# Kernel tuning notes

Hardware: AMD Instinct MI355X
Metric: run time of the kernel (lower is better)

The kernel has to match this reference:

```python
import jax, jax.numpy as jnp
import numpy as np

# Static config (matches init_kwargs / chosen geometry)
DIM, HEADS, WS, SHIFT = 96, 3, 7, 3
H, W = 56, 56
B = 64
N = WS * WS
HID = int(DIM * 4.0)
EPS = 1e-5


def _rel_tables():
    # relative_coords_table: (1, 2*WS-1, 2*WS-1, 2), log-spaced coords in [-1,1]
    c = np.arange(-(WS - 1), WS, dtype=np.float32)
    tab = np.stack(np.meshgrid(c, c, indexing='ij'), axis=-1)[None]
    tab = tab / (WS - 1) * 8.0
    tab = np.sign(tab) * np.log2(np.abs(tab) + 1.0) / np.log2(8.0)
    # relative_position_index: (N, N) int
    coords = np.stack(np.meshgrid(np.arange(WS), np.arange(WS), indexing='ij'))
    cf = coords.reshape(2, -1)
    rel = (cf[:, :, None] - cf[:, None, :]).transpose(1, 2, 0).astype(np.int64)
    rel[..., 0] += WS - 1
    rel[..., 1] += WS - 1
    rel[..., 0] *= 2 * WS - 1
    return jnp.asarray(tab), jnp.asarray(rel.sum(-1))

_TABLE, _RPI = _rel_tables()


def _shift_mask():
    # standard SW-MSA mask: (num_windows, N, N), 0 / -100
    img = np.zeros((1, H, W, 1), dtype=np.float32)
    cnt = 0
    segs = (slice(0, -WS), slice(-WS, -SHIFT), slice(-SHIFT, None))
    for hs in segs:
        for ws_ in segs:
            img[:, hs, ws_, :] = cnt
            cnt += 1
    mw = img.reshape(1, H // WS, WS, W // WS, WS, 1).transpose(0, 1, 3, 2, 4, 5).reshape(-1, N)
    am = mw[:, None, :] - mw[:, :, None]
    return jnp.asarray(np.where(am != 0, -100.0, 0.0).astype(np.float32))


def _ln(x, g, b):
    mu = x.mean(-1, keepdims=True)
    var = x.var(-1, keepdims=True)
    return (x - mu) * jax.lax.rsqrt(var + EPS) * g + b


def setup_inputs() -> dict:
    key = jax.random.key(0)
    ks = jax.random.split(key, 8)
    s = 0.02
    return {
        'x': jax.random.normal(ks[0], (B, H * W, DIM), jnp.float32),
        'attn_mask': _shift_mask(),
        'qkv_w': jax.random.normal(ks[1], (3 * DIM, DIM), jnp.float32) * s,
        'q_bias': jnp.zeros((DIM,), jnp.float32),
        'v_bias': jnp.zeros((DIM,), jnp.float32),
        'logit_scale': jnp.full((HEADS, 1, 1), np.log(10.0), jnp.float32),
        'cpb_w1': jax.random.normal(ks[2], (512, 2), jnp.float32) * s,
        'cpb_b1': jnp.zeros((512,), jnp.float32),
        'cpb_w2': jax.random.normal(ks[3], (HEADS, 512), jnp.float32) * s,
        'proj_w': jax.random.normal(ks[4], (DIM, DIM), jnp.float32) * s,
        'proj_b': jnp.zeros((DIM,), jnp.float32),
        'norm1_g': jnp.ones((DIM,), jnp.float32),
        'norm1_b': jnp.zeros((DIM,), jnp.float32),
        'fc1_w': jax.random.normal(ks[5], (HID, DIM), jnp.float32) * s,
        'fc1_b': jnp.zeros((HID,), jnp.float32),
        'fc2_w': jax.random.normal(ks[6], (DIM, HID), jnp.float32) * s,
        'fc2_b': jnp.zeros((DIM,), jnp.float32),
        'norm2_g': jnp.ones((DIM,), jnp.float32),
        'norm2_b': jnp.zeros((DIM,), jnp.float32),
    }


def reference(x, attn_mask, qkv_w, q_bias, v_bias, logit_scale, cpb_w1, cpb_b1,
              cpb_w2, proj_w, proj_b, norm1_g, norm1_b, fc1_w, fc1_b, fc2_w,
              fc2_b, norm2_g, norm2_b):
    Bx, L, C = x.shape
    d = C // HEADS
    nH, nWd = H // WS, W // WS
    shortcut = x

    xi = x.reshape(Bx, H, W, C)
    xi = jnp.roll(xi, (-SHIFT, -SHIFT), axis=(1, 2))
    # window partition -> (Bx*nH*nWd, N, C)
    xw = xi.reshape(Bx, nH, WS, nWd, WS, C).transpose(0, 1, 3, 2, 4, 5).reshape(-1, N, C)

    # qkv with q/v bias only (k bias fixed to zero)
    qkv_bias = jnp.concatenate([q_bias, jnp.zeros_like(v_bias), v_bias])
    qkv = (xw @ qkv_w.T + qkv_bias).reshape(-1, N, 3, HEADS, d).transpose(2, 0, 3, 1, 4)
    q, k, v = qkv[0], qkv[1], qkv[2]  # (B_, h, N, d)

    # cosine attention with clamped learnable temperature
    qn = q / jnp.maximum(jnp.linalg.norm(q, axis=-1, keepdims=True), 1e-12)
    kn = k / jnp.maximum(jnp.linalg.norm(k, axis=-1, keepdims=True), 1e-12)
    attn = jnp.einsum('bhnd,bhmd->bhnm', qn, kn)
    scale = jnp.exp(jnp.minimum(logit_scale, jnp.log(jnp.float32(100.0))))
    attn = attn * scale

    # continuous relative position bias via cpb_mlp
    tab = jax.nn.gelu(_TABLE @ cpb_w1.T + cpb_b1, approximate=False) @ cpb_w2.T
    tab = tab.reshape(-1, HEADS)
    rpb = tab[_RPI.reshape(-1)].reshape(N, N, HEADS).transpose(2, 0, 1)
    attn = attn + (16.0 * jax.nn.sigmoid(rpb))[None]

    # shift mask
    nWin = attn_mask.shape[0]
    attn = attn.reshape(-1, nWin, HEADS, N, N) + attn_mask[None, :, None]
    attn = jax.nn.softmax(attn.reshape(-1, HEADS, N, N), axis=-1)

    out = jnp.einsum('bhnm,bhmd->bnhd', attn, v).reshape(-1, N, C)
    out = out @ proj_w.T + proj_b

    # window reverse + un-shift
    out = out.reshape(Bx, nH, nWd, WS, WS, C).transpose(0, 1, 3, 2, 4, 5).reshape(Bx, H, W, C)
    out = jnp.roll(out, (SHIFT, SHIFT), axis=(1, 2)).reshape(Bx, L, C)

    # SwinV2 post-norm residuals
    x1 = shortcut + _ln(out, norm1_g, norm1_b)
    h = jax.nn.gelu(x1 @ fc1_w.T + fc1_b, approximate=False) @ fc2_w.T + fc2_b
    return x1 + _ln(h, norm2_g, norm2_b)
```

## Files before the change

### kernel.cpp

```cpp
#include <hip/hip_runtime.h>
#include <math.h>

#define BATCH 64
#define HW 56
#define CDIM 96
#define NHEADS 3
#define WSZ 7
#define NTOK 49
#define SHIFT_ 3
#define NWIN_TOT 4096
#define HID 384
#define NTOKENS (BATCH * HW * HW)
#define LN100 4.6051702f

typedef __attribute__((ext_vector_type(8))) short bf16x8;
typedef __attribute__((ext_vector_type(8))) _Float16 f16x8;
typedef __attribute__((ext_vector_type(4))) float f32x4;

__device__ inline f32x4 mfma16(bf16x8 a, bf16x8 b, f32x4 c) {
  return __builtin_amdgcn_mfma_f32_16x16x32_bf16(a, b, c, 0, 0, 0);
}
__device__ inline f32x4 mfma16h(f16x8 a, f16x8 b, f32x4 c) {
  return __builtin_amdgcn_mfma_f32_16x16x32_f16(a, b, c, 0, 0, 0);
}

__device__ inline unsigned short f2b(float f) {
  unsigned u = __float_as_uint(f);
  unsigned r = (u + 0x7FFFu + ((u >> 16) & 1u)) >> 16;
  return (unsigned short)r;
}
__device__ inline float blo(unsigned u) { return __uint_as_float(u << 16); }
__device__ inline float bhi(unsigned u) { return __uint_as_float(u & 0xFFFF0000u); }
__device__ inline unsigned packb(float a, float b) {
  return (unsigned)f2b(a) | ((unsigned)f2b(b) << 16);
}
__device__ inline float gelu_f(float v) {
  float a = fabsf(v) * 0.70710678118654752f;
  float t = 1.0f / fmaf(a, 0.3275911f, 1.0f);
  float p = t * fmaf(t, fmaf(t, fmaf(t, fmaf(t, 1.061405429f, -1.453152027f),
                                     1.421413741f), -0.284496736f), 0.254829592f);
  float er = 1.0f - p * __expf(-a * a);
  er = (v < 0.f) ? -er : er;
  return 0.5f * v * (1.0f + er);
}

__global__ __launch_bounds__(256) void wconv2_kernel(
    const float* __restrict__ qkv_w, const float* __restrict__ fc1_w,
    const float* __restrict__ fc2_w, const float* __restrict__ proj_w,
    unsigned* __restrict__ qkvf, unsigned* __restrict__ w1f,
    unsigned* __restrict__ w2f, unsigned* __restrict__ pwf) {
  int T = blockIdx.x * 256 + threadIdx.x;
  if (T < 3456) {
    int tk = T >> 6, l = T & 63;
    int n = tk / 3, ks = tk - n * 3;
    int o = n * 16 + (l & 15);
    const float* src = qkv_w + o * 96 + ks * 32 + (l >> 4) * 8;
    uint4 d;
    d.x = packb(src[0], src[1]); d.y = packb(src[2], src[3]);
    d.z = packb(src[4], src[5]); d.w = packb(src[6], src[7]);
    *(uint4*)&qkvf[(size_t)(tk * 64 + l) * 4] = d;
    return;
  }
  T -= 3456;
  if (T < 4608) {
    int tk = T >> 6, l = T & 63;
    int n = tk / 3, ks = tk - n * 3;
    int o = n * 16 + (l & 15);
    const float* src = fc1_w + o * 96 + ks * 32 + (l >> 4) * 8;
    uint4 d;
    d.x = packb(src[0], src[1]); d.y = packb(src[2], src[3]);
    d.z = packb(src[4], src[5]); d.w = packb(src[6], src[7]);
    *(uint4*)&w1f[(size_t)(tk * 64 + l) * 4] = d;
    return;
  }
  T -= 4608;
  if (T < 4608) {
    int tk = T >> 6, l = T & 63;
    int n = tk / 12, ks = tk - n * 12;
    int o = n * 16 + (l & 15);
    const float* src = fc2_w + o * 384 + ks * 32 + (l >> 4) * 8;
    uint4 d;
    d.x = packb(src[0], src[1]); d.y = packb(src[2], src[3]);
    d.z = packb(src[4], src[5]); d.w = packb(src[6], src[7]);
    *(uint4*)&w2f[(size_t)(tk * 64 + l) * 4] = d;
    return;
  }
  T -= 4608;
  if (T < 1152) {
    int tk = T >> 6, l = T & 63;
    int n = tk / 3, ks = tk - n * 3;
    int o = n * 16 + (l & 15);
    const float* src = proj_w + o * 96 + ks * 32 + (l >> 4) * 8;
    uint4 d;
    d.x = packb(src[0], src[1]); d.y = packb(src[2], src[3]);
    d.z = packb(src[4], src[5]); d.w = packb(src[6], src[7]);
    *(uint4*)&pwf[(size_t)(tk * 64 + l) * 4] = d;
  }
}

__global__ __launch_bounds__(512) void cpb_table_kernel(
    const float* __restrict__ w1, const float* __restrict__ b1,
    const float* __restrict__ w2, float* __restrict__ tabout) {
  int tid = threadIdx.x;
  if (tid >= 169 * 3) return;
  int e = tid / 3, h = tid - e * 3;
  int i = e / 13, j = e - i * 13;
  float ti = (float)(i - 6) * (8.0f / 6.0f);
  float tj = (float)(j - 6) * (8.0f / 6.0f);
  float sx = (ti > 0.f) ? 1.f : (ti < 0.f ? -1.f : 0.f);
  float sy = (tj > 0.f) ? 1.f : (tj < 0.f ? -1.f : 0.f);
  float tx = sx * log2f(fabsf(ti) + 1.f) * (1.0f / 3.0f);
  float ty = sy * log2f(fabsf(tj) + 1.f) * (1.0f / 3.0f);
  float acc = 0.f;
  for (int jj = 0; jj < 512; ++jj) {
    float hv = tx * w1[jj * 2 + 0] + ty * w1[jj * 2 + 1] + b1[jj];
    float g = 0.5f * hv * (1.f + erff(hv * 0.70710678118654752f));
    acc += g * w2[h * 512 + jj];
  }
  tabout[e * 3 + h] = acc;
}

__global__ __launch_bounds__(256) void bias_kernel(
    const float* __restrict__ tabout, float* __restrict__ bias16) {
  int idx = blockIdx.x * 256 + threadIdx.x;
  if (idx >= NHEADS * NTOK * NTOK) return;
  int h = idx / (NTOK * NTOK);
  int rem = idx - h * NTOK * NTOK;
  int i = rem / NTOK, j = rem - i * NTOK;
  int ri = (i / WSZ) - (j / WSZ) + 6;
  int ci = (i % WSZ) - (j % WSZ) + 6;
  int e = ri * 13 + ci;
  float v = tabout[e * 3 + h];
  bias16[idx] = 16.f / (1.f + expf(-v));
}

__global__ __launch_bounds__(256) void qkv_mfma_kernel(
    const float* __restrict__ x, const unsigned* __restrict__ qkvf,
    const float* __restrict__ q_bias, const float* __restrict__ v_bias,
    const float* __restrict__ logit_scale,
    unsigned* __restrict__ qws, unsigned* __restrict__ kws,
    unsigned* __restrict__ vws) {
  __shared__ unsigned xa[64 * 52];
  int tid = threadIdx.x, lane = tid & 63, wv = tid >> 6;
  size_t tok0 = (size_t)blockIdx.x * 64;

  for (int idx = tid; idx < 3072; idx += 256) {
    int t = idx / 48, c2 = idx - t * 48;
    const float2 s = *(const float2*)(x + (tok0 + t) * 96 + c2 * 2);
    xa[t * 52 + c2] = packb(s.x, s.y);
  }
  __syncthreads();

  int c15 = lane & 15, q4 = lane >> 4;
  bf16x8 afr[3];
  #pragma unroll
  for (int k = 0; k < 3; ++k)
    afr[k] = *(const bf16x8*)&xa[(wv * 16 + c15) * 52 + k * 16 + q4 * 4];

  f32x4 acc[18];
  #pragma unroll
  for (int n = 0; n < 18; ++n) acc[n] = f32x4{0.f, 0.f, 0.f, 0.f};
  #pragma unroll
  for (int n = 0; n < 18; ++n) {
    #pragma unroll
    for (int k = 0; k < 3; ++k) {
      bf16x8 b = *(const bf16x8*)&qkvf[(size_t)((n * 3 + k) * 64 + lane) * 4];
      acc[n] = mfma16(afr[k], b, acc[n]);
    }
  }

  int tokr0 = (int)tok0 + wv * 16 + q4 * 4;
  #pragma unroll
  for (int h = 0; h < 3; ++h) {
    float sc = expf(fminf(logit_scale[h], LN100));
    {
      f32x4 a0 = acc[2 * h], a1 = acc[2 * h + 1];
      float b0 = q_bias[h * 32 + c15], b1 = q_bias[h * 32 + 16 + c15];
      unsigned pk[8];
      #pragma unroll
      for (int i = 0; i < 4; ++i) {
        float va = a0[i] + b0, vb = a1[i] + b1;
        float ss = va * va + vb * vb;
        ss += __shfl_xor(ss, 1, 64); ss += __shfl_xor(ss, 2, 64);
        ss += __shfl_xor(ss, 4, 64); ss += __shfl_xor(ss, 8, 64);
        float inv = sc / fmaxf(sqrtf(ss), 1e-12f);
        va *= inv; vb *= inv;
        float pa = __shfl_xor(va, 1, 64), pb = __shfl_xor(vb, 1, 64);
        pk[i] = packb(va, pa); pk[4 + i] = packb(vb, pb);
      }
      if (!(lane & 1)) {
        int dw0 = c15 >> 1;
        #pragma unroll
        for (int i = 0; i < 4; ++i) {
          size_t base = ((size_t)(tokr0 + i) * 3 + h) * 16;
          qws[base + dw0] = pk[i];
          qws[base + 8 + dw0] = pk[4 + i];
        }
      }
    }
    {
      f32x4 a0 = acc[6 + 2 * h], a1 = acc[7 + 2 * h];
      unsigned pk[8];
      #pragma unroll
      for (int i = 0; i < 4; ++i) {
        float va = a0[i], vb = a1[i];
        float ss = va * va + vb * vb;
        ss += __shfl_xor(ss, 1, 64); ss += __shfl_xor(ss, 2, 64);
        ss += __shfl_xor(ss, 4, 64); ss += __shfl_xor(ss, 8, 64);
        float inv = 1.f / fmaxf(sqrtf(ss), 1e-12f);
        va *= inv; vb *= inv;
        float pa = __shfl_xor(va, 1, 64), pb = __shfl_xor(vb, 1, 64);
        pk[i] = packb(va, pa); pk[4 + i] = packb(vb, pb);
      }
      if (!(lane & 1)) {
        int dw0 = c15 >> 1;
        #pragma unroll
        for (int i = 0; i < 4; ++i) {
          size_t base = ((size_t)(tokr0 + i) * 3 + h) * 16;
          kws[base + dw0] = pk[i];
          kws[base + 8 + dw0] = pk[4 + i];
        }
      }
    }
    {
      f32x4 a0 = acc[12 + 2 * h], a1 = acc[13 + 2 * h];
      float b0 = v_bias[h * 32 + c15], b1 = v_bias[h * 32 + 16 + c15];
      unsigned pk[8];
      #pragma unroll
      for (int i = 0; i < 4; ++i) {
        float va = a0[i] + b0, vb = a1[i] + b1;
        float pa = __shfl_xor(va, 1, 64), pb = __shfl_xor(vb, 1, 64);
        pk[i] = packb(va, pa); pk[4 + i] = packb(vb, pb);
      }
      if (!(lane & 1)) {
        int dw0 = c15 >> 1;
        #pragma unroll
        for (int i = 0; i < 4; ++i) {
          size_t base = ((size_t)(tokr0 + i) * 3 + h) * 16;
          vws[base + dw0] = pk[i];
          vws[base + 8 + dw0] = pk[4 + i];
        }
      }
    }
  }
}

__global__ __launch_bounds__(256) void attn_fused_kernel(
    const unsigned* __restrict__ qws, const unsigned* __restrict__ kws,
    const unsigned* __restrict__ vws, const float* __restrict__ bias16,
    const float* __restrict__ mask, const unsigned* __restrict__ pwf,
    const float* __restrict__ proj_b, const float* __restrict__ x,
    const float* __restrict__ n1g, const float* __restrict__ n1b,
    float* __restrict__ out) {
  __shared__ __align__(16) unsigned smem[12992];
  _Float16* VtS  = (_Float16*)smem;
  _Float16* Ph   = (_Float16*)((char*)smem + 13824);
  unsigned* obuf = (unsigned*)((char*)smem + 38400);
  int*      toks = (int*)((char*)smem + 51712);
  float*    ybuf = (float*)smem;

  int tid = threadIdx.x, lane = tid & 63, wv = tid >> 6;
  int c15 = lane & 15, q4 = lane >> 4;
  int win = blockIdx.x;
  int b = win >> 6, wi = win & 63, wh = wi >> 3, wcx = wi & 7;

  if (tid < 64) {
    int t = tid < 49 ? tid : 48;
    int tr = (t * 9363) >> 16, tc = t - tr * 7;
    int R = wh * 7 + tr + SHIFT_; if (R >= HW) R -= HW;
    int C = wcx * 7 + tc + SHIFT_; if (C >= HW) C -= HW;
    toks[tid] = b * 3136 + R * 56 + C;
  }
  __syncthreads();

  bf16x8 qf[4], kf[4];
  if (wv < 3) {
    #pragma unroll
    for (int m = 0; m < 4; ++m)
      qf[m] = *(const bf16x8*)&qws[((size_t)toks[m * 16 + c15] * 3 + wv) * 16 + q4 * 4];
    #pragma unroll
    for (int n = 0; n < 4; ++n)
      kf[n] = *(const bf16x8*)&kws[((size_t)toks[n * 16 + c15] * 3 + wv) * 16 + q4 * 4];
  }

  for (int idx = tid; idx < 768; idx += 256) {
    int h2 = idx >> 8, rem = idx & 255;
    int t = rem >> 2, dg = rem & 3;
    uint4 v4 = *(const uint4*)&vws[((size_t)toks[t] * 3 + h2) * 16 + dg * 4];
    _Float16* dst = &VtS[h2 * 2304 + (dg * 8) * 72 + t];
    dst[0 * 72] = (_Float16)blo(v4.x); dst[1 * 72] = (_Float16)bhi(v4.x);
    dst[2 * 72] = (_Float16)blo(v4.y); dst[3 * 72] = (_Float16)bhi(v4.y);
    dst[4 * 72] = (_Float16)blo(v4.z); dst[5 * 72] = (_Float16)bhi(v4.z);
    dst[6 * 72] = (_Float16)blo(v4.w); dst[7 * 72] = (_Float16)bhi(v4.w);
  }
  __syncthreads();

  if (wv < 3) {
    int h = wv;
    f32x4 s[4][4];
    #pragma unroll
    for (int m = 0; m < 4; ++m)
      #pragma unroll
      for (int n = 0; n < 4; ++n)
        s[m][n] = mfma16(qf[m], kf[n], f32x4{0.f, 0.f, 0.f, 0.f});

    const float* bsl = bias16 + h * 2401;
    const float* msl = mask + (size_t)wi * 2401;
    #pragma unroll
    for (int m = 0; m < 4; ++m) {
      #pragma unroll
      for (int i = 0; i < 4; ++i) {
        int rw = m * 16 + 4 * q4 + i;
        if (rw < 49) {
          const float* br = bsl + rw * 49;
          const float* mr = msl + rw * 49;
          #pragma unroll
          for (int n = 0; n < 4; ++n) {
            int j = n * 16 + c15;
            s[m][n][i] = (j < 49) ? (s[m][n][i] + br[j] + mr[j]) : -1e30f;
          }
        } else {
          #pragma unroll
          for (int n = 0; n < 4; ++n)
            if (n * 16 + c15 >= 49) s[m][n][i] = -1e30f;
        }
      }
    }

    #pragma unroll
    for (int m = 0; m < 4; ++m) {
      #pragma unroll
      for (int i = 0; i < 4; ++i) {
        float mx = fmaxf(fmaxf(s[m][0][i], s[m][1][i]), fmaxf(s[m][2][i], s[m][3][i]));
        mx = fmaxf(mx, __shfl_xor(mx, 1, 64)); mx = fmaxf(mx, __shfl_xor(mx, 2, 64));
        mx = fmaxf(mx, __shfl_xor(mx, 4, 64)); mx = fmaxf(mx, __shfl_xor(mx, 8, 64));
        float sum = 0.f;
        #pragma unroll
        for (int n = 0; n < 4; ++n) { float e = __expf(s[m][n][i] - mx); s[m][n][i] = e; sum += e; }
        sum += __shfl_xor(sum, 1, 64); sum += __shfl_xor(sum, 2, 64);
        sum += __shfl_xor(sum, 4, 64); sum += __shfl_xor(sum, 8, 64);
        float inv = 1.f / sum;
        #pragma unroll
        for (int n = 0; n < 4; ++n) s[m][n][i] *= inv;
      }
    }

    #pragma unroll
    for (int m = 0; m < 4; ++m)
      #pragma unroll
      for (int n = 0; n < 4; ++n) {
        int gw = n * 2 + (c15 >> 3);
        #pragma unroll
        for (int i = 0; i < 4; ++i) {
          int row = m * 16 + 4 * q4 + i;
          int gp = gw ^ (row & 7);
          Ph[h * 4096 + row * 64 + gp * 8 + (c15 & 7)] = (_Float16)s[m][n][i];
        }
      }
    asm volatile("s_waitcnt lgkmcnt(0)" ::: "memory");
    __builtin_amdgcn_sched_barrier(0);

    f32x4 o[4][2];
    #pragma unroll
    for (int m = 0; m < 4; ++m)
      #pragma unroll
      for (int n2 = 0; n2 < 2; ++n2) o[m][n2] = f32x4{0.f, 0.f, 0.f, 0.f};
    #pragma unroll
    for (int ks = 0; ks < 2; ++ks) {
      f16x8 pa[4];
      #pragma unroll
      for (int m = 0; m < 4; ++m) {
        int row = m * 16 + c15;
        int gp = (ks * 4 + q4) ^ (c15 & 7);
        pa[m] = *(const f16x8*)&Ph[h * 4096 + row * 64 + gp * 8];
      }
      #pragma unroll
      for (int n2 = 0; n2 < 2; ++n2) {
        f16x8 vb = *(const f16x8*)&VtS[h * 2304 + (n2 * 16 + c15) * 72 + ks * 32 + q4 * 8];
        #pragma unroll
        for (int m = 0; m < 4; ++m) o[m][n2] = mfma16h(pa[m], vb, o[m][n2]);
      }
    }

    #pragma unroll
    for (int m = 0; m < 4; ++m)
      #pragma unroll
      for (int n2 = 0; n2 < 2; ++n2)
        #pragma unroll
        for (int i = 0; i < 4; ++i) {
          float ov = o[m][n2][i];
          float on = __shfl_xor(ov, 1, 64);
          if (!(lane & 1))
            obuf[(m * 16 + 4 * q4 + i) * 52 + h * 16 + n2 * 8 + (c15 >> 1)] = packb(ov, on);
        }
  }
  __syncthreads();

  bf16x8 oa[3];
  #pragma unroll
  for (int ks = 0; ks < 3; ++ks)
    oa[ks] = *(const bf16x8*)&obuf[(wv * 16 + c15) * 52 + ks * 16 + q4 * 4];
  f32x4 pr[6];
  #pragma unroll
  for (int n = 0; n < 6; ++n) pr[n] = f32x4{0.f, 0.f, 0.f, 0.f};
  #pragma unroll
  for (int n = 0; n < 6; ++n)
    #pragma unroll
    for (int ks = 0; ks < 3; ++ks) {
      bf16x8 bfr = *(const bf16x8*)&pwf[(size_t)((n * 3 + ks) * 64 + lane) * 4];
      pr[n] = mfma16(oa[ks], bfr, pr[n]);
    }

  #pragma unroll
  for (int n = 0; n < 6; ++n) {
    int col = n * 16 + c15;
    float bo = proj_b[col];
    #pragma unroll
    for (int i = 0; i < 4; ++i)
      ybuf[(wv * 16 + 4 * q4 + i) * 100 + col] = pr[n][i] + bo;
  }
  __syncthreads();

  int t = tid >> 2, pp = tid & 3;
  if (t < 49) {
    const float* yrow = ybuf + t * 100 + pp * 24;
    float s1 = 0.f;
    #pragma unroll
    for (int c = 0; c < 24; ++c) s1 += yrow[c];
    s1 += __shfl_xor(s1, 1, 64); s1 += __shfl_xor(s1, 2, 64);
    float mu = s1 * (1.f / 96.f);
    float v2 = 0.f;
    #pragma unroll
    for (int c = 0; c < 24; ++c) { float d = yrow[c] - mu; v2 += d * d; }
    v2 += __shfl_xor(v2, 1, 64); v2 += __shfl_xor(v2, 2, 64);
    float rs = rsqrtf(v2 * (1.f / 96.f) + 1e-5f);
    size_t base = (size_t)toks[t] * 96 + pp * 24;
    #pragma unroll
    for (int c4 = 0; c4 < 6; ++c4) {
      float4 xv = *(const float4*)(x + base + c4 * 4);
      float4 gv = *(const float4*)(n1g + pp * 24 + c4 * 4);
      float4 bv = *(const float4*)(n1b + pp * 24 + c4 * 4);
      float4 ov;
      ov.x = xv.x + (yrow[c4 * 4 + 0] - mu) * rs * gv.x + bv.x;
      ov.y = xv.y + (yrow[c4 * 4 + 1] - mu) * rs * gv.y + bv.y;
      ov.z = xv.z + (yrow[c4 * 4 + 2] - mu) * rs * gv.z + bv.z;
      ov.w = xv.w + (yrow[c4 * 4 + 3] - mu) * rs * gv.w + bv.w;
      *(float4*)(out + base + c4 * 4) = ov;
    }
  }
}

__global__ __launch_bounds__(256) void mlp_mfma_kernel(
    const unsigned* __restrict__ w1f, const float* __restrict__ fc1_b,
    const unsigned* __restrict__ w2f, const float* __restrict__ fc2_b,
    const float* __restrict__ n2g, const float* __restrict__ n2b,
    float* __restrict__ xio) {
  __shared__ __align__(16) unsigned mlpbuf[12544];
  __shared__ float mu_s[64], rs_s[64];
  unsigned* xa  = mlpbuf;
  unsigned* hid = mlpbuf;
  float*   ybuf = (float*)mlpbuf;
  int tid = threadIdx.x, lane = tid & 63, wv = tid >> 6;
  int c15 = lane & 15, q4 = lane >> 4;
  size_t tok0 = (size_t)blockIdx.x * 64;

  for (int idx = tid; idx < 3072; idx += 256) {
    int t = idx / 48, c2 = idx - t * 48;
    const float2 s = *(const float2*)(xio + (tok0 + t) * 96 + c2 * 2);
    xa[t * 52 + c2] = packb(s.x, s.y);
  }
  __syncthreads();

  bf16x8 afr[4][3];
  #pragma unroll
  for (int m = 0; m < 4; ++m)
    #pragma unroll
    for (int k = 0; k < 3; ++k)
      afr[m][k] = *(const bf16x8*)&xa[(m * 16 + c15) * 52 + k * 16 + q4 * 4];
  __syncthreads();

  f32x4 acc[4][6];
  #pragma unroll
  for (int m = 0; m < 4; ++m)
    #pragma unroll
    for (int n = 0; n < 6; ++n) acc[m][n] = f32x4{0.f, 0.f, 0.f, 0.f};
  #pragma unroll
  for (int n = 0; n < 6; ++n) {
    #pragma unroll
    for (int k = 0; k < 3; ++k) {
      bf16x8 b = *(const bf16x8*)&w1f[(size_t)(((6 * wv + n) * 3 + k) * 64 + lane) * 4];
      #pragma unroll
      for (int m = 0; m < 4; ++m) acc[m][n] = mfma16(afr[m][k], b, acc[m][n]);
    }
  }
  unsigned short* hidb = (unsigned short*)hid;
  #pragma unroll
  for (int n = 0; n < 6; ++n) {
    int col = (6 * wv + n) * 16 + c15;
    float bo = fc1_b[col];
    #pragma unroll
    for (int m = 0; m < 4; ++m) {
      #pragma unroll
      for (int i = 0; i < 4; ++i) {
        float g = gelu_f(acc[m][n][i] + bo);
        hidb[(m * 16 + q4 * 4 + i) * 392 + col] = f2b(g);
      }
    }
  }
  __syncthreads();

  f32x4 acc2[6];
  #pragma unroll
  for (int n = 0; n < 6; ++n) acc2[n] = f32x4{0.f, 0.f, 0.f, 0.f};
  #pragma unroll
  for (int k = 0; k < 12; ++k) {
    bf16x8 a = *(const bf16x8*)&hid[(wv * 16 + c15) * 196 + k * 16 + q4 * 4];
    #pragma unroll
    for (int n = 0; n < 6; ++n) {
      bf16x8 b = *(const bf16x8*)&w2f[(size_t)((n * 12 + k) * 64 + lane) * 4];
      acc2[n] = mfma16(a, b, acc2[n]);
    }
  }
  __syncthreads();

  #pragma unroll
  for (int n = 0; n < 6; ++n) {
    int col = n * 16 + c15;
    float bo = fc2_b[col];
    #pragma unroll
    for (int i = 0; i < 4; ++i)
      ybuf[(wv * 16 + q4 * 4 + i) * 100 + col] = acc2[n][i] + bo;
  }
  __syncthreads();

  {
    int t = tid >> 2, p = tid & 3;
    const float* row = ybuf + t * 100 + p * 24;
    float s = 0.f, s2 = 0.f;
    for (int c = 0; c < 24; ++c) { float v = row[c]; s += v; s2 += v * v; }
    s += __shfl_xor(s, 1, 64); s2 += __shfl_xor(s2, 1, 64);
    s += __shfl_xor(s, 2, 64); s2 += __shfl_xor(s2, 2, 64);
    if (p == 0) {
      float mu = s * (1.f / 96.f);
      float var = s2 * (1.f / 96.f) - mu * mu;
      mu_s[t] = mu;
      rs_s[t] = rsqrtf(fmaxf(var, 0.f) + 1e-5f);
    }
  }
  __syncthreads();

  for (int idx = tid; idx < 6144; idx += 256) {
    int t = idx / 96, c = idx - t * 96;
    float y = ybuf[t * 100 + c];
    xio[tok0 * 96 + idx] += (y - mu_s[t]) * rs_s[t] * n2g[c] + n2b[c];
  }
}

extern "C" void kernel_launch(void* const* d_in, const int* in_sizes, int n_in,
                              void* d_out, int out_size, void* d_ws, size_t ws_size,
                              hipStream_t stream) {
  const float* x           = (const float*)d_in[0];
  const float* attn_mask   = (const float*)d_in[1];
  const float* qkv_w       = (const float*)d_in[2];
  const float* q_bias      = (const float*)d_in[3];
  const float* v_bias      = (const float*)d_in[4];
  const float* logit_scale = (const float*)d_in[5];
  const float* cpb_w1      = (const float*)d_in[6];
  const float* cpb_b1      = (const float*)d_in[7];
  const float* cpb_w2      = (const float*)d_in[8];
  const float* proj_w      = (const float*)d_in[9];
  const float* proj_b      = (const float*)d_in[10];
  const float* n1g         = (const float*)d_in[11];
  const float* n1b         = (const float*)d_in[12];
  const float* fc1_w       = (const float*)d_in[13];
  const float* fc1_b       = (const float*)d_in[14];
  const float* fc2_w       = (const float*)d_in[15];
  const float* fc2_b       = (const float*)d_in[16];
  const float* n2g         = (const float*)d_in[17];
  const float* n2b         = (const float*)d_in[18];
  float* out = (float*)d_out;

  float* tab     = (float*)d_ws;
  float* bias16  = tab + 512;
  unsigned* qkvf = (unsigned*)(bias16 + 7296);
  unsigned* w1f  = qkvf + 13824;
  unsigned* w2f  = w1f + 18432;
  unsigned* pwf  = w2f + 18432;
  unsigned* qws  = pwf + 4608;
  unsigned* kws  = qws + 9633792;
  unsigned* vws  = kws + 9633792;

  wconv2_kernel<<<54, 256, 0, stream>>>(qkv_w, fc1_w, fc2_w, proj_w,
                                        qkvf, w1f, w2f, pwf);
  cpb_table_kernel<<<1, 512, 0, stream>>>(cpb_w1, cpb_b1, cpb_w2, tab);
  bias_kernel<<<(NHEADS * NTOK * NTOK + 255) / 256, 256, 0, stream>>>(tab, bias16);
  qkv_mfma_kernel<<<NTOKENS / 64, 256, 0, stream>>>(x, qkvf, q_bias, v_bias,
                                                    logit_scale, qws, kws, vws);
  attn_fused_kernel<<<NWIN_TOT, 256, 0, stream>>>(qws, kws, vws, bias16, attn_mask,
                                                  pwf, proj_b, x, n1g, n1b, out);
  mlp_mfma_kernel<<<NTOKENS / 64, 256, 0, stream>>>(w1f, fc1_b, w2f, fc2_b,
                                                    n2g, n2b, out);
}
```

Before: 546.6 us.

## Shrink attention LDS footprint, repack P as f16 pairs, vectorize MLP epilogue

```diff
diff --git a/kernel.cpp b/kernel.cpp
--- a/kernel.cpp
+++ b/kernel.cpp
@@ -33,6 +33,11 @@
 __device__ inline float bhi(unsigned u) { return __uint_as_float(u & 0xFFFF0000u); }
 __device__ inline unsigned packb(float a, float b) {
   return (unsigned)f2b(a) | ((unsigned)f2b(b) << 16);
+}
+__device__ inline unsigned packh(float a, float b) {
+  _Float16 ha = (_Float16)a, hb = (_Float16)b;
+  unsigned short ua = *(unsigned short*)&ha, ub = *(unsigned short*)&hb;
+  return (unsigned)ua | ((unsigned)ub << 16);
 }
 __device__ inline float gelu_f(float v) {
   float a = fabsf(v) * 0.70710678118654752f;
@@ -252,12 +257,13 @@
     const float* __restrict__ proj_b, const float* __restrict__ x,
     const float* __restrict__ n1g, const float* __restrict__ n1b,
     float* __restrict__ out) {
-  __shared__ __align__(16) unsigned smem[12992];
+  __shared__ __align__(16) unsigned smem[10432];
   _Float16* VtS  = (_Float16*)smem;
+  unsigned* obuf = (unsigned*)smem;
   _Float16* Ph   = (_Float16*)((char*)smem + 13824);
-  unsigned* obuf = (unsigned*)((char*)smem + 38400);
-  int*      toks = (int*)((char*)smem + 51712);
-  float*    ybuf = (float*)smem;
+  unsigned* Phd  = (unsigned*)((char*)smem + 13824);
+  float*    ybuf = (float*)((char*)smem + 13824);
+  int*      toks = (int*)((char*)smem + 41472);
 
   int tid = threadIdx.x, lane = tid & 63, wv = tid >> 6;
   int c15 = lane & 15, q4 = lane >> 4;
@@ -294,6 +300,12 @@
     dst[6 * 72] = (_Float16)blo(v4.w); dst[7 * 72] = (_Float16)bhi(v4.w);
   }
   __syncthreads();
+
+  f32x4 o[4][2];
+  #pragma unroll
+  for (int m = 0; m < 4; ++m)
+    #pragma unroll
+    for (int n2 = 0; n2 < 2; ++n2) o[m][n2] = f32x4{0.f, 0.f, 0.f, 0.f};
 
   if (wv < 3) {
     int h = wv;
@@ -348,32 +360,25 @@
     #pragma unroll
     for (int m = 0; m < 4; ++m)
       #pragma unroll
-      for (int n = 0; n < 4; ++n) {
-        int gw = n * 2 + (c15 >> 3);
+      for (int n = 0; n < 4; ++n)
         #pragma unroll
         for (int i = 0; i < 4; ++i) {
-          int row = m * 16 + 4 * q4 + i;
-          int gp = gw ^ (row & 7);
-          Ph[h * 4096 + row * 64 + gp * 8 + (c15 & 7)] = (_Float16)s[m][n][i];
+          float pv = s[m][n][i];
+          float pn = __shfl_xor(pv, 1, 64);
+          if (!(lane & 1)) {
+            int row = m * 16 + 4 * q4 + i;
+            Phd[h * 2304 + row * 36 + n * 8 + (c15 >> 1)] = packh(pv, pn);
+          }
         }
-      }
     asm volatile("s_waitcnt lgkmcnt(0)" ::: "memory");
     __builtin_amdgcn_sched_barrier(0);
 
-    f32x4 o[4][2];
-    #pragma unroll
-    for (int m = 0; m < 4; ++m)
-      #pragma unroll
-      for (int n2 = 0; n2 < 2; ++n2) o[m][n2] = f32x4{0.f, 0.f, 0.f, 0.f};
     #pragma unroll
     for (int ks = 0; ks < 2; ++ks) {
       f16x8 pa[4];
       #pragma unroll
-      for (int m = 0; m < 4; ++m) {
-        int row = m * 16 + c15;
-        int gp = (ks * 4 + q4) ^ (c15 & 7);
-        pa[m] = *(const f16x8*)&Ph[h * 4096 + row * 64 + gp * 8];
-      }
+      for (int m = 0; m < 4; ++m)
+        pa[m] = *(const f16x8*)&Ph[h * 4608 + (m * 16 + c15) * 72 + ks * 32 + q4 * 8];
       #pragma unroll
       for (int n2 = 0; n2 < 2; ++n2) {
         f16x8 vb = *(const f16x8*)&VtS[h * 2304 + (n2 * 16 + c15) * 72 + ks * 32 + q4 * 8];
@@ -381,7 +386,11 @@
         for (int m = 0; m < 4; ++m) o[m][n2] = mfma16h(pa[m], vb, o[m][n2]);
       }
     }
-
+  }
+  __syncthreads();
+
+  if (wv < 3) {
+    int h = wv;
     #pragma unroll
     for (int m = 0; m < 4; ++m)
       #pragma unroll
@@ -455,11 +464,9 @@
     const unsigned* __restrict__ w2f, const float* __restrict__ fc2_b,
     const float* __restrict__ n2g, const float* __restrict__ n2b,
     float* __restrict__ xio) {
-  __shared__ __align__(16) unsigned mlpbuf[12544];
+  __shared__ unsigned xa[64 * 52];
+  __shared__ unsigned hid[64 * 196];
   __shared__ float mu_s[64], rs_s[64];
-  unsigned* xa  = mlpbuf;
-  unsigned* hid = mlpbuf;
-  float*   ybuf = (float*)mlpbuf;
   int tid = threadIdx.x, lane = tid & 63, wv = tid >> 6;
   int c15 = lane & 15, q4 = lane >> 4;
   size_t tok0 = (size_t)blockIdx.x * 64;
@@ -477,8 +484,6 @@
     #pragma unroll
     for (int k = 0; k < 3; ++k)
       afr[m][k] = *(const bf16x8*)&xa[(m * 16 + c15) * 52 + k * 16 + q4 * 4];
-  __syncthreads();
-
   f32x4 acc[4][6];
   #pragma unroll
   for (int m = 0; m < 4; ++m)
@@ -523,6 +528,7 @@
   }
   __syncthreads();
 
+  float* ybuf = (float*)hid;
   #pragma unroll
   for (int n = 0; n < 6; ++n) {
     int col = n * 16 + c15;
@@ -549,10 +555,20 @@
   }
   __syncthreads();
 
-  for (int idx = tid; idx < 6144; idx += 256) {
-    int t = idx / 96, c = idx - t * 96;
-    float y = ybuf[t * 100 + c];
-    xio[tok0 * 96 + idx] += (y - mu_s[t]) * rs_s[t] * n2g[c] + n2b[c];
+  for (int idx = tid; idx < 1536; idx += 256) {
+    int t = idx / 24, c4 = (idx - t * 24) * 4;
+    float mu = mu_s[t], rs = rs_s[t];
+    float4 y4 = *(float4*)&ybuf[t * 100 + c4];
+    float4 g4 = *(const float4*)&n2g[c4];
+    float4 b4 = *(const float4*)&n2b[c4];
+    float* gp = &xio[tok0 * 96 + t * 96 + c4];
+    float4 x4 = *(const float4*)gp;
+    float4 ov;
+    ov.x = x4.x + (y4.x - mu) * rs * g4.x + b4.x;
+    ov.y = x4.y + (y4.y - mu) * rs * g4.y + b4.y;
+    ov.z = x4.z + (y4.z - mu) * rs * g4.z + b4.z;
+    ov.w = x4.w + (y4.w - mu) * rs * g4.w + b4.w;
+    *(float4*)gp = ov;
   }
 }
 
```

Measured after the change: 498.1 us. -8.9%, faster.
